# Kernel tuning notes

Measured on AMD Instinct MI355X. Metric: run time of the kernel, lower is better.

Reference implementation:

```python
import jax, jax.numpy as jnp
import numpy as np

S, D, H = 4096, 2048, 16
HD = D // H

def setup_inputs() -> dict:
    key = jax.random.key(0)
    ks = jax.random.split(key, 9)
    s = 1.0 / np.sqrt(D)
    return {
        "hidden_states": jax.random.normal(ks[0], (S, D), jnp.float32),
        "Wq": jax.random.uniform(ks[1], (D, D), jnp.float32, -s, s),
        "bq": jax.random.uniform(ks[2], (D,), jnp.float32, -s, s),
        "Wk": jax.random.uniform(ks[3], (D, D), jnp.float32, -s, s),
        "bk": jax.random.uniform(ks[4], (D,), jnp.float32, -s, s),
        "Wv": jax.random.uniform(ks[5], (D, D), jnp.float32, -s, s),
        "bv": jax.random.uniform(ks[6], (D,), jnp.float32, -s, s),
        "Wo": jax.random.uniform(ks[7], (D, D), jnp.float32, -s, s),
        "bo": jax.random.uniform(ks[8], (D,), jnp.float32, -s, s),
    }

def reference(hidden_states, Wq, bq, Wk, bk, Wv, bv, Wo, bo):
    seq = hidden_states.shape[0]
    # projections (torch Linear: x @ W.T + b)
    q = (hidden_states @ Wq.T + bq).reshape(seq, H, HD).transpose(1, 0, 2)  # [H,S,hd]
    k = (hidden_states @ Wk.T + bk).reshape(seq, H, HD).transpose(1, 0, 2)
    v = (hidden_states @ Wv.T + bv).reshape(seq, H, HD).transpose(1, 0, 2)
    scale = 1.0 / np.sqrt(HD).astype(np.float32)
    qk = jnp.einsum('hqd,hkd->hqk', q, k) * scale  # [H,S,S]
    causal = jnp.tril(jnp.ones((seq, seq), bool))
    qk = jnp.where(causal, qk, -jnp.inf)
    attn = jax.nn.softmax(qk, axis=-1)
    out = jnp.einsum('hqk,hkd->hqd', attn, v)  # [H,S,hd]
    out = out.transpose(1, 0, 2).reshape(seq, D)
    return out @ Wo.T + bo
```

## Files before the change

### kernel.cpp

```cpp
#include <hip/hip_runtime.h>
#include <stdint.h>

#define S_LEN 4096
#define D_DIM 2048
#define NHEAD 16
#define HDIM  128

typedef short bf16x8 __attribute__((ext_vector_type(8)));
typedef float f32x4  __attribute__((ext_vector_type(4)));
typedef float f32x16 __attribute__((ext_vector_type(16)));

__device__ __forceinline__ unsigned short f2bf(float x) {
  union { float f; unsigned u; } v; v.f = x;
  unsigned r = v.u + 0x7FFFu + ((v.u >> 16) & 1u);
  return (unsigned short)(r >> 16);
}

__device__ __forceinline__ float bf2f(unsigned short s) {
  union { unsigned u; float f; } v; v.u = ((unsigned)s) << 16;
  return v.f;
}

__device__ __forceinline__ unsigned cvtpk_bf16(float lo, float hi_) {
  unsigned r;
  asm("v_cvt_pk_bf16_f32 %0, %1, %2" : "=v"(r) : "v"(lo), "v"(hi_));
  return r;
}

__device__ __forceinline__ void gload_lds16(const void* g, void* l) {
  __builtin_amdgcn_global_load_lds(
      (const __attribute__((address_space(1))) unsigned int*)g,
      (__attribute__((address_space(3))) unsigned int*)l, 16, 0, 0);
}

__global__ __launch_bounds__(256) void cvt_all(
    const float* __restrict__ X, const float* __restrict__ Wq,
    const float* __restrict__ Wk, const float* __restrict__ Wv,
    const float* __restrict__ Wo, unsigned short* __restrict__ out) {
  const size_t DD = (size_t)D_DIM * D_DIM;
  size_t i = ((size_t)blockIdx.x * 256 + threadIdx.x) * 8;
  const float* src; size_t off;
  if (i < 2 * DD)      { src = X;  off = i; }
  else if (i < 3 * DD) { src = Wq; off = i - 2 * DD; }
  else if (i < 4 * DD) { src = Wk; off = i - 3 * DD; }
  else if (i < 5 * DD) { src = Wv; off = i - 4 * DD; }
  else                 { src = Wo; off = i - 5 * DD; }
  float4 a = *(const float4*)(src + off);
  float4 b = *(const float4*)(src + off + 4);
  union { unsigned short s[8]; bf16x8 v; } o;
  o.s[0] = f2bf(a.x); o.s[1] = f2bf(a.y); o.s[2] = f2bf(a.z); o.s[3] = f2bf(a.w);
  o.s[4] = f2bf(b.x); o.s[5] = f2bf(b.y); o.s[6] = f2bf(b.z); o.s[7] = f2bf(b.w);
  *(bf16x8*)(out + i) = o.v;
}

__global__ __launch_bounds__(256, 2) void gemm_qkv(
    const unsigned short* __restrict__ A, const unsigned short* __restrict__ W,
    const float* __restrict__ bq, const float* __restrict__ bk,
    const float* __restrict__ bv, unsigned short* __restrict__ Q,
    unsigned short* __restrict__ Ko, unsigned short* __restrict__ V,
    float qsc) {
  __shared__ __attribute__((aligned(16))) unsigned short As[128 * 32];
  __shared__ __attribute__((aligned(16))) unsigned short Bs[128 * 32];
  const int m0 = blockIdx.y * 128, n0 = blockIdx.x * 128;
  const int tid = threadIdx.x, lane = tid & 63, wv = tid >> 6;
  const int wm = wv >> 1, wn = wv & 1;
  const int rA = lane & 15, kb = (lane >> 4) * 8;
  const int K = D_DIM;

  f32x4 acc[4][4];
#pragma unroll
  for (int i = 0; i < 4; ++i)
#pragma unroll
    for (int j = 0; j < 4; ++j)
#pragma unroll
      for (int r = 0; r < 4; ++r) acc[i][j][r] = 0.f;

  for (int k0 = 0; k0 < K; k0 += 32) {
    __syncthreads();
#pragma unroll
    for (int p = 0; p < 2; ++p) {
      const int rr = (wv * 2 + p) * 16 + (lane >> 2);
      const int cc = lane & 3;
      gload_lds16(A + (size_t)(m0 + rr) * K + k0 + cc * 8, As + (wv * 2 + p) * 512);
      gload_lds16(W + (size_t)(n0 + rr) * K + k0 + cc * 8, Bs + (wv * 2 + p) * 512);
    }
    __syncthreads();
    bf16x8 af[4], bfr[4];
#pragma unroll
    for (int i = 0; i < 4; ++i)
      af[i] = *(const bf16x8*)(As + (wm * 64 + i * 16 + rA) * 32 + kb);
#pragma unroll
    for (int j = 0; j < 4; ++j)
      bfr[j] = *(const bf16x8*)(Bs + (wn * 64 + j * 16 + rA) * 32 + kb);
#pragma unroll
    for (int i = 0; i < 4; ++i)
#pragma unroll
      for (int j = 0; j < 4; ++j)
        acc[i][j] = __builtin_amdgcn_mfma_f32_16x16x32_bf16(af[i], bfr[j], acc[i][j], 0, 0, 0);
  }

  const int cR = (lane >> 4) * 4, cC = lane & 15;
#pragma unroll
  for (int j = 0; j < 4; ++j) {
    const int col = n0 + wn * 64 + j * 16 + cC;
    const int seg = col >> 11, cl = col & 2047;
    const float* bp = (seg == 0) ? bq : (seg == 1) ? bk : bv;
    unsigned short* op = (seg == 0) ? Q : (seg == 1) ? Ko : V;
    const float es = (seg == 0) ? qsc : 1.0f;
    const float bvv = bp[cl];
#pragma unroll
    for (int i = 0; i < 4; ++i) {
      const int row0 = m0 + wm * 64 + i * 16 + cR;
#pragma unroll
      for (int r = 0; r < 4; ++r)
        op[(size_t)(row0 + r) * D_DIM + cl] = f2bf((acc[i][j][r] + bvv) * es);
    }
  }
}

__global__ __launch_bounds__(256, 2) void gemm_bt_f32(
    const unsigned short* __restrict__ A, const unsigned short* __restrict__ B,
    const float* __restrict__ bias, float* __restrict__ Cout,
    int M, int N, int K) {
  __shared__ __attribute__((aligned(16))) unsigned short As[128 * 32];
  __shared__ __attribute__((aligned(16))) unsigned short Bs[128 * 32];
  const int m0 = blockIdx.y * 128, n0 = blockIdx.x * 128;
  const int tid = threadIdx.x, lane = tid & 63, wv = tid >> 6;
  const int wm = wv >> 1, wn = wv & 1;
  const int rA = lane & 15, kb = (lane >> 4) * 8;

  f32x4 acc[4][4];
#pragma unroll
  for (int i = 0; i < 4; ++i)
#pragma unroll
    for (int j = 0; j < 4; ++j)
#pragma unroll
      for (int r = 0; r < 4; ++r) acc[i][j][r] = 0.f;

  for (int k0 = 0; k0 < K; k0 += 32) {
    __syncthreads();
#pragma unroll
    for (int p = 0; p < 2; ++p) {
      const int rr = (wv * 2 + p) * 16 + (lane >> 2);
      const int cc = lane & 3;
      gload_lds16(A + (size_t)(m0 + rr) * K + k0 + cc * 8, As + (wv * 2 + p) * 512);
      gload_lds16(B + (size_t)(n0 + rr) * K + k0 + cc * 8, Bs + (wv * 2 + p) * 512);
    }
    __syncthreads();
    bf16x8 af[4], bfr[4];
#pragma unroll
    for (int i = 0; i < 4; ++i)
      af[i] = *(const bf16x8*)(As + (wm * 64 + i * 16 + rA) * 32 + kb);
#pragma unroll
    for (int j = 0; j < 4; ++j)
      bfr[j] = *(const bf16x8*)(Bs + (wn * 64 + j * 16 + rA) * 32 + kb);
#pragma unroll
    for (int i = 0; i < 4; ++i)
#pragma unroll
      for (int j = 0; j < 4; ++j)
        acc[i][j] = __builtin_amdgcn_mfma_f32_16x16x32_bf16(af[i], bfr[j], acc[i][j], 0, 0, 0);
  }

  const int cR = (lane >> 4) * 4, cC = lane & 15;
#pragma unroll
  for (int j = 0; j < 4; ++j) {
    const int col = n0 + wn * 64 + j * 16 + cC;
    const float bvv = bias[col];
#pragma unroll
    for (int i = 0; i < 4; ++i) {
      const int row0 = m0 + wm * 64 + i * 16 + cR;
#pragma unroll
      for (int r = 0; r < 4; ++r)
        Cout[(size_t)(row0 + r) * N + col] = acc[i][j][r] + bvv;
    }
  }
}

__global__ __launch_bounds__(512, 2) void attn_part(
    const unsigned short* __restrict__ Qb, const unsigned short* __restrict__ Kb,
    const unsigned short* __restrict__ Vb, unsigned short* __restrict__ Opart,
    float* __restrict__ ML) {
  __shared__ __attribute__((aligned(16))) unsigned short Ks[64 * 128];
  __shared__ __attribute__((aligned(16))) unsigned short Vt[128 * 64];
  const int bid = blockIdx.x;
  const int xcd = bid & 7, rb = bid >> 3;
  const int d = (rb < 32) ? rb : 95 - rb;
  const int qp = 15 - (d >> 2);
  const int h = (xcd << 1) | (d & 1);
  const int hf = (d >> 1) & 1;
  const int q0 = qp * 256;
  const int u2 = (h * 16 + qp) * 2 + hf;
  const int tid = threadIdx.x, lane = tid & 63, wv = tid >> 6;
  const int qc = lane & 31, hi = lane >> 5;
  const int q0w = q0 + wv * 32;
  const int myq = q0w + qc;
  const int kp = tid & 31, hb = (tid >> 5) * 8;

  bf16x8 qf[8];
#pragma unroll
  for (int sl = 0; sl < 8; ++sl)
    qf[sl] = *(const bf16x8*)(Qb + (size_t)myq * D_DIM + h * HDIM + sl * 16 + hi * 8);

  f32x16 oacc[4];
#pragma unroll
  for (int nf = 0; nf < 4; ++nf)
#pragma unroll
    for (int r = 0; r < 16; ++r) oacc[nf][r] = 0.f;
  float mh = -3.0e38f, l = 0.f;

  const int ntil = 2 * (qp + 1);
  const int klo = hf * ntil, khi = klo + ntil;
  const int wqmax = q0w + 31;

  for (int kt = klo; kt < khi; ++kt) {
    const int k0 = kt * 64;
    __syncthreads();
#pragma unroll
    for (int p = 0; p < 2; ++p) {
      const int ob = wv * 2048 + p * 1024;
      const int o = ob + lane * 16;
      const int r = o >> 8, c = (o >> 4) & 15;
      gload_lds16(Kb + (size_t)(k0 + r) * D_DIM + h * HDIM + (c ^ (r & 7)) * 8,
                  Ks + ob / 2);
    }
    {
      const unsigned short* s0 = Vb + (size_t)(k0 + 2 * kp) * D_DIM + h * HDIM + hb;
      union { uint4 u[2]; unsigned short s[16]; } t;
      t.u[0] = *(const uint4*)s0;
      t.u[1] = *(const uint4*)(s0 + D_DIM);
#pragma unroll
      for (int w = 0; w < 8; ++w) {
        const int hd = hb + w;
        const unsigned val = (unsigned)t.s[w] | ((unsigned)t.s[8 + w] << 16);
        *(unsigned*)((char*)Vt + hd * 128 + (((kp >> 2) ^ (hd & 7)) << 4) + ((kp & 3) << 2)) = val;
      }
    }
    __syncthreads();
    if (k0 > wqmax) continue;

    f32x16 sacc[2];
#pragma unroll
    for (int kb = 0; kb < 2; ++kb)
#pragma unroll
      for (int r = 0; r < 16; ++r) sacc[kb][r] = 0.f;
    __builtin_amdgcn_s_setprio(1);
#pragma unroll
    for (int sl = 0; sl < 8; ++sl) {
#pragma unroll
      for (int kb = 0; kb < 2; ++kb) {
        const int row = kb * 32 + qc;
        bf16x8 kfr = *(const bf16x8*)((const char*)Ks + row * 256 +
                                      (((2 * sl + hi) ^ (qc & 7)) << 4));
        sacc[kb] = __builtin_amdgcn_mfma_f32_32x32x16_bf16(kfr, qf[sl], sacc[kb], 0, 0, 0);
      }
    }
    __builtin_amdgcn_s_setprio(0);

    const bool needmask = (k0 + 63 > q0w);
    if (needmask) {
      const int dq = myq - k0;
#pragma unroll
      for (int kb = 0; kb < 2; ++kb)
#pragma unroll
        for (int r = 0; r < 16; ++r) {
          const int kk = kb * 32 + (r & 3) + 8 * (r >> 2) + 4 * hi;
          if (kk > dq) sacc[kb][r] = -3.0e38f;
        }
    }
    float mx0[8];
#pragma unroll
    for (int t = 0; t < 8; ++t)
      mx0[t] = fmaxf(fmaxf(sacc[0][t], sacc[0][t + 8]),
                     fmaxf(sacc[1][t], sacc[1][t + 8]));
    float mx = fmaxf(fmaxf(fmaxf(mx0[0], mx0[1]), fmaxf(mx0[2], mx0[3])),
                     fmaxf(fmaxf(mx0[4], mx0[5]), fmaxf(mx0[6], mx0[7])));
    mx = fmaxf(mx, __shfl_xor(mx, 32));
    if (!__all(mx <= mh + 11.5f)) {
      const float mnew = fmaxf(mh, mx);
      const float corr = exp2f(mh - mnew);
      mh = mnew;
      l *= corr;
#pragma unroll
      for (int r = 0; r < 16; ++r) {
        const float cr = __shfl(corr, (r & 3) + 8 * (r >> 2) + 4 * hi);
#pragma unroll
        for (int nf = 0; nf < 4; ++nf) oacc[nf][r] *= cr;
      }
    }
    float rs = 0.f;
#pragma unroll
    for (int kb = 0; kb < 2; ++kb)
#pragma unroll
      for (int r = 0; r < 16; ++r) {
        const float p = exp2f(sacc[kb][r] - mh);
        sacc[kb][r] = p;
        rs += p;
      }
    rs += __shfl_xor(rs, 32);
    l += rs;

    bf16x8 pa[4];
#pragma unroll
    for (int kb = 0; kb < 2; ++kb)
#pragma unroll
      for (int s = 0; s < 2; ++s) {
        const int b = s * 8;
        unsigned pk0 = cvtpk_bf16(sacc[kb][b + 0], sacc[kb][b + 1]);
        unsigned pk1 = cvtpk_bf16(sacc[kb][b + 2], sacc[kb][b + 3]);
        unsigned pk2 = cvtpk_bf16(sacc[kb][b + 4], sacc[kb][b + 5]);
        unsigned pk3 = cvtpk_bf16(sacc[kb][b + 6], sacc[kb][b + 7]);
        const unsigned sw0 = (unsigned)__shfl_xor((int)pk0, 32);
        const unsigned sw1 = (unsigned)__shfl_xor((int)pk1, 32);
        const unsigned sw2 = (unsigned)__shfl_xor((int)pk2, 32);
        const unsigned sw3 = (unsigned)__shfl_xor((int)pk3, 32);
        union { unsigned u[4]; bf16x8 v; } f;
        if (hi) { f.u[0] = sw2; f.u[1] = sw3; f.u[2] = pk2; f.u[3] = pk3; }
        else    { f.u[0] = pk0; f.u[1] = pk1; f.u[2] = sw0; f.u[3] = sw1; }
        pa[kb * 2 + s] = f.v;
      }

    __builtin_amdgcn_s_setprio(1);
#pragma unroll
    for (int nf = 0; nf < 4; ++nf) {
      const int hd = 32 * nf + qc;
#pragma unroll
      for (int ks = 0; ks < 4; ++ks) {
        bf16x8 vf = *(const bf16x8*)((const char*)Vt + hd * 128 +
                                     (((2 * ks + hi) ^ (qc & 7)) << 4));
        oacc[nf] = __builtin_amdgcn_mfma_f32_32x32x16_bf16(pa[ks], vf, oacc[nf], 0, 0, 0);
      }
    }
    __builtin_amdgcn_s_setprio(0);
  }

  unsigned short* ob = Opart + (size_t)u2 * 32768;
#pragma unroll
  for (int r = 0; r < 16; ++r) {
    const int rl = wv * 32 + (r & 3) + 8 * (r >> 2) + 4 * hi;
#pragma unroll
    for (int nf = 0; nf < 4; ++nf)
      ob[rl * 128 + 32 * nf + qc] = f2bf(oacc[nf][r]);
  }
  if (hi == 0) {
    ML[(size_t)u2 * 512 + wv * 32 + qc] = mh;
    ML[(size_t)u2 * 512 + 256 + wv * 32 + qc] = l;
  }
}

__global__ __launch_bounds__(256) void attn_combine(
    const unsigned short* __restrict__ Opart, const float* __restrict__ ML,
    unsigned short* __restrict__ Ob) {
  const int u = blockIdx.x;
  const int h = u >> 4, qp = u & 15;
  const int tid = threadIdx.x;
  const unsigned short* p1 = Opart + (size_t)(u * 2 + 0) * 32768;
  const unsigned short* p2 = Opart + (size_t)(u * 2 + 1) * 32768;
  const float* ml1 = ML + (size_t)(u * 2 + 0) * 512;
  const float* ml2 = ML + (size_t)(u * 2 + 1) * 512;
#pragma unroll
  for (int i = 0; i < 16; ++i) {
    const int chunk = i * 256 + tid;
    const int row = chunk >> 4, col = (chunk & 15) * 8;
    const float m1 = ml1[row], l1 = ml1[256 + row];
    const float m2 = ml2[row], l2 = ml2[256 + row];
    const float M = fmaxf(m1, m2);
    const float a1 = exp2f(m1 - M), a2 = exp2f(m2 - M);
    const float inv = 1.f / (a1 * l1 + a2 * l2);
    bf16x8 v1 = *(const bf16x8*)(p1 + chunk * 8);
    bf16x8 v2 = *(const bf16x8*)(p2 + chunk * 8);
    union { unsigned short s[8]; bf16x8 v; } o;
#pragma unroll
    for (int e = 0; e < 8; ++e)
      o.s[e] = f2bf((bf2f((unsigned short)v1[e]) * a1 +
                     bf2f((unsigned short)v2[e]) * a2) * inv);
    *(bf16x8*)(Ob + (size_t)(qp * 256 + row) * D_DIM + h * HDIM + col) = o.v;
  }
}

extern "C" void kernel_launch(void* const* d_in, const int* in_sizes, int n_in,
                              void* d_out, int out_size, void* d_ws, size_t ws_size,
                              hipStream_t stream) {
  const float* X  = (const float*)d_in[0];
  const float* Wq = (const float*)d_in[1];
  const float* bq = (const float*)d_in[2];
  const float* Wk = (const float*)d_in[3];
  const float* bk = (const float*)d_in[4];
  const float* Wv = (const float*)d_in[5];
  const float* bv = (const float*)d_in[6];
  const float* Wo = (const float*)d_in[7];
  const float* bo = (const float*)d_in[8];
  float* out = (float*)d_out;

  unsigned short* ws = (unsigned short*)d_ws;
  const size_t SD = (size_t)S_LEN * D_DIM;
  const size_t DD = (size_t)D_DIM * D_DIM;
  unsigned short* Xb  = ws;
  unsigned short* Wqb = Xb + SD;
  unsigned short* Wob = Wqb + 3 * DD;
  unsigned short* Qb  = Wob + DD;
  unsigned short* Kb  = Qb + SD;
  unsigned short* Vb  = Kb + SD;
  unsigned short* AOb = Vb + SD;
  unsigned short* Opart = ws;
  float* ML = (float*)(ws + SD + 2 * DD);

  cvt_all<<<(int)(6 * DD / 8 / 256), 256, 0, stream>>>(X, Wq, Wk, Wv, Wo, Xb);

  const float qsc = 0.08838834764831845f * 1.4426950408889634f;
  gemm_qkv<<<dim3(48, 32), 256, 0, stream>>>(Xb, Wqb, bq, bk, bv, Qb, Kb, Vb, qsc);

  attn_part<<<dim3(512), 512, 0, stream>>>(Qb, Kb, Vb, Opart, ML);
  attn_combine<<<dim3(256), 256, 0, stream>>>(Opart, ML, AOb);

  gemm_bt_f32<<<dim3(16, 32), 256, 0, stream>>>(AOb, Wob, bo, out, S_LEN, D_DIM, D_DIM);
}
```

Measured before the change: 340.1 us.

## Halve attention query tile to 128 rows with 4 waves, doubling block count

The attention kernel now uses 128-query blocks with 4 waves (256 threads) instead of 256-query blocks with 8 waves, giving 1024 blocks in place of 512. Each thread loads more K/V per tile to fill shared memory. The combine kernel is reshaped to one row-half per thread with 512 blocks. The aim is finer causal granularity, so less masked work and better load balance across CUs. The cost is that each loaded K/V tile is reused by fewer queries, and the previous balanced block-to-work mapping is replaced by a simpler descending order.

Measured after the change: 321.8 us. 5.4% less time.

```diff
diff --git a/kernel.cpp b/kernel.cpp
--- a/kernel.cpp
+++ b/kernel.cpp
@@ -176,25 +176,23 @@
   }
 }
 
-__global__ __launch_bounds__(512, 2) void attn_part(
+__global__ __launch_bounds__(256, 2) void attn_part(
     const unsigned short* __restrict__ Qb, const unsigned short* __restrict__ Kb,
     const unsigned short* __restrict__ Vb, unsigned short* __restrict__ Opart,
     float* __restrict__ ML) {
   __shared__ __attribute__((aligned(16))) unsigned short Ks[64 * 128];
   __shared__ __attribute__((aligned(16))) unsigned short Vt[128 * 64];
   const int bid = blockIdx.x;
-  const int xcd = bid & 7, rb = bid >> 3;
-  const int d = (rb < 32) ? rb : 95 - rb;
-  const int qp = 15 - (d >> 2);
-  const int h = (xcd << 1) | (d & 1);
-  const int hf = (d >> 1) & 1;
-  const int q0 = qp * 256;
-  const int u2 = (h * 16 + qp) * 2 + hf;
+  const int h  = ((bid & 7) << 1) | ((bid >> 3) & 1);
+  const int hf = (bid >> 4) & 1;
+  const int qi = 31 - (bid >> 5);
+  const int q0 = qi * 128;
+  const int u2 = (h * 32 + qi) * 2 + hf;
   const int tid = threadIdx.x, lane = tid & 63, wv = tid >> 6;
   const int qc = lane & 31, hi = lane >> 5;
   const int q0w = q0 + wv * 32;
   const int myq = q0w + qc;
-  const int kp = tid & 31, hb = (tid >> 5) * 8;
+  const int kp = tid & 31, hb = (tid >> 5) * 16;
 
   bf16x8 qf[8];
 #pragma unroll
@@ -208,16 +206,15 @@
     for (int r = 0; r < 16; ++r) oacc[nf][r] = 0.f;
   float mh = -3.0e38f, l = 0.f;
 
-  const int ntil = 2 * (qp + 1);
-  const int klo = hf * ntil, khi = klo + ntil;
+  const int klo = hf * (qi + 1), khi = klo + qi + 1;
   const int wqmax = q0w + 31;
 
   for (int kt = klo; kt < khi; ++kt) {
     const int k0 = kt * 64;
     __syncthreads();
 #pragma unroll
-    for (int p = 0; p < 2; ++p) {
-      const int ob = wv * 2048 + p * 1024;
+    for (int p = 0; p < 4; ++p) {
+      const int ob = wv * 4096 + p * 1024;
       const int o = ob + lane * 16;
       const int r = o >> 8, c = (o >> 4) & 15;
       gload_lds16(Kb + (size_t)(k0 + r) * D_DIM + h * HDIM + (c ^ (r & 7)) * 8,
@@ -225,13 +222,13 @@
     }
     {
       const unsigned short* s0 = Vb + (size_t)(k0 + 2 * kp) * D_DIM + h * HDIM + hb;
-      union { uint4 u[2]; unsigned short s[16]; } t;
-      t.u[0] = *(const uint4*)s0;
-      t.u[1] = *(const uint4*)(s0 + D_DIM);
-#pragma unroll
-      for (int w = 0; w < 8; ++w) {
+      union { uint4 u[4]; unsigned short s[32]; } t;
+      t.u[0] = *(const uint4*)s0;           t.u[1] = *(const uint4*)(s0 + 8);
+      t.u[2] = *(const uint4*)(s0 + D_DIM); t.u[3] = *(const uint4*)(s0 + D_DIM + 8);
+#pragma unroll
+      for (int w = 0; w < 16; ++w) {
         const int hd = hb + w;
-        const unsigned val = (unsigned)t.s[w] | ((unsigned)t.s[8 + w] << 16);
+        const unsigned val = (unsigned)t.s[w] | ((unsigned)t.s[16 + w] << 16);
         *(unsigned*)((char*)Vt + hd * 128 + (((kp >> 2) ^ (hd & 7)) << 4) + ((kp & 3) << 2)) = val;
       }
     }
@@ -333,7 +330,7 @@
     __builtin_amdgcn_s_setprio(0);
   }
 
-  unsigned short* ob = Opart + (size_t)u2 * 32768;
+  unsigned short* ob = Opart + (size_t)u2 * 16384;
 #pragma unroll
   for (int r = 0; r < 16; ++r) {
     const int rl = wv * 32 + (r & 3) + 8 * (r >> 2) + 4 * hi;
@@ -342,8 +339,8 @@
       ob[rl * 128 + 32 * nf + qc] = f2bf(oacc[nf][r]);
   }
   if (hi == 0) {
-    ML[(size_t)u2 * 512 + wv * 32 + qc] = mh;
-    ML[(size_t)u2 * 512 + 256 + wv * 32 + qc] = l;
+    ML[(size_t)u2 * 256 + wv * 32 + qc] = mh;
+    ML[(size_t)u2 * 256 + 128 + wv * 32 + qc] = l;
   }
 }
 
@@ -351,29 +348,29 @@
     const unsigned short* __restrict__ Opart, const float* __restrict__ ML,
     unsigned short* __restrict__ Ob) {
   const int u = blockIdx.x;
-  const int h = u >> 4, qp = u & 15;
+  const int h = u >> 5, qi = u & 31;
   const int tid = threadIdx.x;
-  const unsigned short* p1 = Opart + (size_t)(u * 2 + 0) * 32768;
-  const unsigned short* p2 = Opart + (size_t)(u * 2 + 1) * 32768;
-  const float* ml1 = ML + (size_t)(u * 2 + 0) * 512;
-  const float* ml2 = ML + (size_t)(u * 2 + 1) * 512;
-#pragma unroll
-  for (int i = 0; i < 16; ++i) {
-    const int chunk = i * 256 + tid;
-    const int row = chunk >> 4, col = (chunk & 15) * 8;
-    const float m1 = ml1[row], l1 = ml1[256 + row];
-    const float m2 = ml2[row], l2 = ml2[256 + row];
-    const float M = fmaxf(m1, m2);
-    const float a1 = exp2f(m1 - M), a2 = exp2f(m2 - M);
-    const float inv = 1.f / (a1 * l1 + a2 * l2);
-    bf16x8 v1 = *(const bf16x8*)(p1 + chunk * 8);
-    bf16x8 v2 = *(const bf16x8*)(p2 + chunk * 8);
-    union { unsigned short s[8]; bf16x8 v; } o;
+  const int row = tid >> 1, c0 = (tid & 1) * 64;
+  const float m1 = ML[(size_t)(u * 2 + 0) * 256 + row];
+  const float l1 = ML[(size_t)(u * 2 + 0) * 256 + 128 + row];
+  const float m2 = ML[(size_t)(u * 2 + 1) * 256 + row];
+  const float l2 = ML[(size_t)(u * 2 + 1) * 256 + 128 + row];
+  const float M  = fmaxf(m1, m2);
+  const float a1 = exp2f(m1 - M), a2 = exp2f(m2 - M);
+  const float inv = 1.f / (a1 * l1 + a2 * l2);
+  const unsigned short* p1 = Opart + (size_t)(u * 2 + 0) * 16384 + row * 128 + c0;
+  const unsigned short* p2 = Opart + (size_t)(u * 2 + 1) * 16384 + row * 128 + c0;
+  unsigned short* o = Ob + (size_t)(qi * 128 + row) * D_DIM + h * HDIM + c0;
+#pragma unroll
+  for (int c = 0; c < 64; c += 8) {
+    bf16x8 v1 = *(const bf16x8*)(p1 + c);
+    bf16x8 v2 = *(const bf16x8*)(p2 + c);
+    union { unsigned short s[8]; bf16x8 v; } out;
 #pragma unroll
     for (int e = 0; e < 8; ++e)
-      o.s[e] = f2bf((bf2f((unsigned short)v1[e]) * a1 +
-                     bf2f((unsigned short)v2[e]) * a2) * inv);
-    *(bf16x8*)(Ob + (size_t)(qp * 256 + row) * D_DIM + h * HDIM + col) = o.v;
+      out.s[e] = f2bf((bf2f((unsigned short)v1[e]) * a1 +
+                       bf2f((unsigned short)v2[e]) * a2) * inv);
+    *(bf16x8*)(o + c) = out.v;
   }
 }
 
@@ -409,8 +406,8 @@
   const float qsc = 0.08838834764831845f * 1.4426950408889634f;
   gemm_qkv<<<dim3(48, 32), 256, 0, stream>>>(Xb, Wqb, bq, bk, bv, Qb, Kb, Vb, qsc);
 
-  attn_part<<<dim3(512), 512, 0, stream>>>(Qb, Kb, Vb, Opart, ML);
-  attn_combine<<<dim3(256), 256, 0, stream>>>(Opart, ML, AOb);
+  attn_part<<<dim3(1024), 256, 0, stream>>>(Qb, Kb, Vb, Opart, ML);
+  attn_combine<<<dim3(512), 256, 0, stream>>>(Opart, ML, AOb);
 
   gemm_bt_f32<<<dim3(16, 32), 256, 0, stream>>>(AOb, Wob, bo, out, S_LEN, D_DIM, D_DIM);
 }
```
